# Optimization experiments

Hardware: AMD Instinct MI355X
Metric: run time of the kernel (lower is better)

## Reference

```python
import jax, jax.numpy as jnp
import numpy as np

N, L, T, D = 64, 196, 32, 512


def setup_inputs() -> dict:
    key = jax.random.key(0)
    ks = jax.random.split(key, 12)
    s = 1.0 / np.sqrt(D)
    return {
        "feature_1": jax.random.normal(ks[0], (N, L, D), jnp.float32),
        "feature_2": jax.random.normal(ks[1], (N, T, D), jnp.float32),
        "w_att": jax.random.normal(ks[2], (D,), jnp.float32) * s,
        "b_att": jnp.zeros((), jnp.float32),
        "n1_w1": jax.random.normal(ks[3], (D, D), jnp.float32) * s,
        "n1_b1": jnp.zeros((D,), jnp.float32),
        "n1_w2": jax.random.normal(ks[4], (D, D), jnp.float32) * s,
        "n1_b2": jnp.zeros((D,), jnp.float32),
        "n2_w1": jax.random.normal(ks[5], (D, D), jnp.float32) * s,
        "n2_b1": jnp.zeros((D,), jnp.float32),
        "n2_w2": jax.random.normal(ks[6], (D, D), jnp.float32) * s,
        "n2_b2": jnp.zeros((D,), jnp.float32),
    }


def _glu(x, w1, b1, w2, b2):
    # tanh(Linear1(x)) * sigmoid(Linear2(x))
    return jnp.tanh(x @ w1 + b1) * jax.nn.sigmoid(x @ w2 + b2)


def reference(feature_1, feature_2, w_att, b_att,
              n1_w1, n1_b1, n1_w2, n1_b2,
              n2_w1, n2_b1, n2_w2, n2_b2):
    f1_emb = _glu(feature_1, n1_w1, n1_b1, n1_w2, n1_b2)  # [N,L,D]
    f2_emb = _glu(feature_2, n2_w1, n2_b1, n2_w2, n2_b2)  # [N,T,D]
    # Attention_1: fc((f1 + f2 broadcast)) == fc(f1) + fc(f2) + bias since fc is linear.
    # Avoids materializing the [N,T,L,D] intermediate while computing identical math.
    s1 = feature_1 @ w_att  # [N,L]
    s2 = feature_2 @ w_att  # [N,T]
    att_logits = s2[:, :, None] + s1[:, None, :] + b_att  # [N,T,L]
    att = jax.nn.softmax(att_logits, axis=2)
    f_hat = jnp.einsum('ntl,nld->ntd', att, feature_1)  # [N,T,D]
    return (f2_emb + f_hat, f1_emb, att)
```

## Files before the change

kernel.cpp:

```cpp
#include <hip/hip_runtime.h>
#include <hip/hip_bf16.h>
#include <cstdint>
#include <cstddef>

#define N_  64
#define L_  196
#define T_  32
#define D_  512
#define LP_ 256
#define ROWS1_ (N_ * L_)
#define ROWS2_ (N_ * T_)
#define NWG1_  ((ROWS1_ / 64) * 4)
#define NWG2_  ((ROWS2_ / 64) * 4)

typedef __attribute__((ext_vector_type(8))) short short8;
typedef __attribute__((ext_vector_type(4))) float f32x4;

__device__ inline unsigned short f2bf(float f) {
  unsigned u = __builtin_bit_cast(unsigned, f);
  u = u + 0x7FFFu + ((u >> 16) & 1u);
  return (unsigned short)(u >> 16);
}

__global__ __launch_bounds__(256)
void cvt_dots(const float* __restrict__ f1, const float* __restrict__ f2,
              const float* __restrict__ w,
              unsigned short* __restrict__ f1b, unsigned short* __restrict__ f2b,
              float* __restrict__ s1, float* __restrict__ s2) {
  int row = blockIdx.x * 4 + (threadIdx.x >> 6);
  int lane = threadIdx.x & 63;
  bool isf1 = row < ROWS1_;
  const float* src = isf1 ? (f1 + (size_t)row * D_) : (f2 + (size_t)(row - ROWS1_) * D_);
  unsigned short* dst = isf1 ? (f1b + (size_t)row * D_) : (f2b + (size_t)(row - ROWS1_) * D_);
  float4 x0 = ((const float4*)src)[lane];
  float4 x1 = ((const float4*)src)[lane + 64];
  float4 w0 = ((const float4*)w)[lane];
  float4 w1 = ((const float4*)w)[lane + 64];
  float d = x0.x * w0.x + x0.y * w0.y + x0.z * w0.z + x0.w * w0.w
          + x1.x * w1.x + x1.y * w1.y + x1.z * w1.z + x1.w * w1.w;
  ushort4 o0, o1;
  o0.x = f2bf(x0.x); o0.y = f2bf(x0.y); o0.z = f2bf(x0.z); o0.w = f2bf(x0.w);
  o1.x = f2bf(x1.x); o1.y = f2bf(x1.y); o1.z = f2bf(x1.z); o1.w = f2bf(x1.w);
  ((ushort4*)dst)[lane] = o0;
  ((ushort4*)dst)[lane + 64] = o1;
  #pragma unroll
  for (int s = 32; s; s >>= 1) d += __shfl_xor(d, s);
  if (lane == 0) {
    if (isf1) s1[row] = d; else s2[row - ROWS1_] = d;
  }
}

__global__ __launch_bounds__(256)
void wt_cvt(const float* __restrict__ w0, const float* __restrict__ w1,
            const float* __restrict__ w2, const float* __restrict__ w3,
            unsigned short* __restrict__ o0, unsigned short* __restrict__ o1,
            unsigned short* __restrict__ o2, unsigned short* __restrict__ o3) {
  const float* W = (blockIdx.y == 0) ? w0 : (blockIdx.y == 1) ? w1 : (blockIdx.y == 2) ? w2 : w3;
  unsigned short* O = (blockIdx.y == 0) ? o0 : (blockIdx.y == 1) ? o1 : (blockIdx.y == 2) ? o2 : o3;
  int k0 = (blockIdx.x >> 3) * 64, n0 = (blockIdx.x & 7) * 64;
  __shared__ float tl[64][65];
  int t = threadIdx.x;
  #pragma unroll
  for (int i = 0; i < 16; i++) {
    int e = t + i * 256;
    int r = e >> 6, c = e & 63;
    tl[r][c] = W[(size_t)(k0 + r) * D_ + n0 + c];
  }
  __syncthreads();
  #pragma unroll
  for (int i = 0; i < 16; i++) {
    int e = t + i * 256;
    int r = e >> 6, c = e & 63;
    O[(size_t)(n0 + r) * D_ + k0 + c] = f2bf(tl[c][r]);
  }
}

__global__ __launch_bounds__(256)
void f1t_cvt(const unsigned short* __restrict__ f1b, unsigned short* __restrict__ f1t) {
  int bi = blockIdx.x;
  int n = bi >> 5, rem = bi & 31;
  int l0 = (rem >> 3) * 64, d0 = (rem & 7) * 64;
  __shared__ unsigned short tl[64][72];
  int t = threadIdx.x;
  #pragma unroll
  for (int i = 0; i < 4; i++) {
    int e = t + i * 256;
    int r = e >> 4, c4 = e & 15;
    int l = l0 + r;
    ushort4 v;
    if (l < L_) v = *(const ushort4*)&f1b[((size_t)n * L_ + l) * D_ + d0 + c4 * 4];
    else { v.x = 0; v.y = 0; v.z = 0; v.w = 0; }
    *(ushort4*)&tl[r][c4 * 4] = v;
  }
  __syncthreads();
  #pragma unroll
  for (int i = 0; i < 4; i++) {
    int e = t + i * 256;
    int r = e >> 4, c4 = e & 15;
    ushort4 o;
    o.x = tl[c4 * 4 + 0][r];
    o.y = tl[c4 * 4 + 1][r];
    o.z = tl[c4 * 4 + 2][r];
    o.w = tl[c4 * 4 + 3][r];
    *(ushort4*)&f1t[((size_t)n * D_ + d0 + r) * LP_ + l0 + c4 * 4] = o;
  }
}

__global__ __launch_bounds__(64)
void softmax_att(const float* __restrict__ s1, const float* __restrict__ s2,
                 const float* __restrict__ b_att, float* __restrict__ att,
                 unsigned short* __restrict__ attb) {
  int b = blockIdx.x;
  int n = b >> 5;
  int lane = threadIdx.x;
  float s2v = s2[b] + b_att[0];
  const float* s1n = s1 + (size_t)n * L_;
  float v[4];
  float mx = -1e30f;
  #pragma unroll
  for (int j = 0; j < 4; j++) {
    int l = lane + j * 64;
    v[j] = (l < L_) ? (s1n[l] + s2v) : -1e30f;
    mx = fmaxf(mx, v[j]);
  }
  #pragma unroll
  for (int s = 32; s; s >>= 1) mx = fmaxf(mx, __shfl_xor(mx, s));
  float sum = 0.f;
  #pragma unroll
  for (int j = 0; j < 4; j++) { v[j] = __expf(v[j] - mx); sum += v[j]; }
  #pragma unroll
  for (int s = 32; s; s >>= 1) sum += __shfl_xor(sum, s);
  float inv = 1.f / sum;
  float* an = att + (size_t)b * L_;
  unsigned short* ab = attb + (size_t)b * LP_;
  #pragma unroll
  for (int j = 0; j < 4; j++) {
    int l = lane + j * 64;
    float p = v[j] * inv;
    if (l < L_) an[l] = p;
    ab[l] = (l < L_) ? f2bf(p) : (unsigned short)0;
  }
}

__global__ __launch_bounds__(256, 3)
void glu_gemm(const unsigned short* __restrict__ Xb1, const unsigned short* __restrict__ Xb2,
              const unsigned short* __restrict__ W1t_1, const unsigned short* __restrict__ W2t_1,
              const unsigned short* __restrict__ W1t_2, const unsigned short* __restrict__ W2t_2,
              const float* __restrict__ b1_1, const float* __restrict__ b2_1,
              const float* __restrict__ b1_2, const float* __restrict__ b2_2,
              float* __restrict__ o1, float* __restrict__ o0) {
  int nwg = gridDim.x;
  int q = nwg >> 3;
  int orig = blockIdx.x;
  int bid = (orig & 7) * q + (orig >> 3);
  const unsigned short *Xb, *W1t, *W2t;
  const float *b1, *b2;
  float* out;
  if (bid < NWG1_) { Xb = Xb1; W1t = W1t_1; W2t = W2t_1; b1 = b1_1; b2 = b2_1; out = o1; }
  else { bid -= NWG1_; Xb = Xb2; W1t = W1t_2; W2t = W2t_2; b1 = b1_2; b2 = b2_2; out = o0; }
  int nt = bid & 3, mt = bid >> 2;
  int m0 = mt * 64, n0 = nt * 128;
  int t = threadIdx.x, lane = t & 63, wave = t >> 6;
  int wr = (wave >> 1) * 32, wc = (wave & 1) * 64;

  __shared__ alignas(16) unsigned short Xs[2][2048];
  __shared__ alignas(16) unsigned short Ws[2][2][4096];

  auto stage = [&](int buf, int k0) {
    {
      int c = t;
      const unsigned short* g = Xb + (size_t)(m0 + (c >> 2)) * D_ + k0 + (c & 3) * 8;
      unsigned short* l = &Xs[buf][(size_t)wave * 512];
      __builtin_amdgcn_global_load_lds((const __attribute__((address_space(1))) unsigned int*)g,
                                       (__attribute__((address_space(3))) unsigned int*)l,
                                       16, 0, 0);
    }
    #pragma unroll
    for (int w = 0; w < 2; w++) {
      const unsigned short* Wt = w ? W2t : W1t;
      #pragma unroll
      for (int i = 0; i < 2; i++) {
        int c = t + i * 256;
        const unsigned short* g = Wt + (size_t)(n0 + (c >> 2)) * D_ + k0 + (c & 3) * 8;
        unsigned short* l = &Ws[buf][w][(size_t)(wave * 64 + i * 256) * 8];
        __builtin_amdgcn_global_load_lds((const __attribute__((address_space(1))) unsigned int*)g,
                                         (__attribute__((address_space(3))) unsigned int*)l,
                                         16, 0, 0);
      }
    }
  };

  f32x4 acc1[2][4], acc2[2][4];
  #pragma unroll
  for (int i = 0; i < 2; i++)
    #pragma unroll
    for (int j = 0; j < 4; j++) { acc1[i][j] = (f32x4)(0.f); acc2[i][j] = (f32x4)(0.f); }

  stage(0, 0);
  int cur = 0;
  int arow = lane & 15, ak = (lane >> 4) * 8;
  for (int ks = 0; ks < 16; ++ks) {
    __syncthreads();
    if (ks < 15) stage(cur ^ 1, (ks + 1) * 32);
    short8 a[2], bf1[4], bf2[4];
    #pragma unroll
    for (int mf = 0; mf < 2; mf++)
      a[mf] = *(const short8*)&Xs[cur][(wr + mf * 16 + arow) * 32 + ak];
    #pragma unroll
    for (int nf = 0; nf < 4; nf++) {
      bf1[nf] = *(const short8*)&Ws[cur][0][(wc + nf * 16 + arow) * 32 + ak];
      bf2[nf] = *(const short8*)&Ws[cur][1][(wc + nf * 16 + arow) * 32 + ak];
    }
    #pragma unroll
    for (int mf = 0; mf < 2; mf++)
      #pragma unroll
      for (int nf = 0; nf < 4; nf++) {
        acc1[mf][nf] = __builtin_amdgcn_mfma_f32_16x16x32_bf16(a[mf], bf1[nf], acc1[mf][nf], 0, 0, 0);
        acc2[mf][nf] = __builtin_amdgcn_mfma_f32_16x16x32_bf16(a[mf], bf2[nf], acc2[mf][nf], 0, 0, 0);
      }
    cur ^= 1;
  }

  int crow = (lane >> 4) * 4, ccol = lane & 15;
  #pragma unroll
  for (int mf = 0; mf < 2; mf++) {
    #pragma unroll
    for (int nf = 0; nf < 4; nf++) {
      int col = n0 + wc + nf * 16 + ccol;
      float bb1 = b1[col], bb2 = b2[col];
      #pragma unroll
      for (int r = 0; r < 4; r++) {
        int row = m0 + wr + mf * 16 + crow + r;
        float z1 = acc1[mf][nf][r] + bb1;
        float z2 = acc2[mf][nf][r] + bb2;
        float th = 1.f - 2.f / (__expf(2.f * z1) + 1.f);
        float sg = 1.f / (1.f + __expf(-z2));
        out[(size_t)row * D_ + col] = th * sg;
      }
    }
  }
}

__global__ __launch_bounds__(256)
void fhat_mfma(const unsigned short* __restrict__ attb,
               const unsigned short* __restrict__ f1t,
               float* __restrict__ out0) {
  int n = blockIdx.x >> 2, dq = blockIdx.x & 3;
  int lane = threadIdx.x & 63, wave = threadIdx.x >> 6;
  int d0 = dq * 128 + wave * 32;
  int arow = lane & 15, ak = (lane >> 4) * 8;
  const unsigned short* A = attb + (size_t)n * T_ * LP_;
  const unsigned short* B = f1t + ((size_t)n * D_ + d0) * LP_;
  f32x4 acc[2][2];
  #pragma unroll
  for (int i = 0; i < 2; i++)
    #pragma unroll
    for (int j = 0; j < 2; j++) acc[i][j] = (f32x4)(0.f);
  #pragma unroll 2
  for (int kk = 0; kk < 8; kk++) {
    int k0 = kk * 32;
    short8 a[2], b[2];
    #pragma unroll
    for (int mt = 0; mt < 2; mt++)
      a[mt] = *(const short8*)&A[(size_t)(mt * 16 + arow) * LP_ + k0 + ak];
    #pragma unroll
    for (int nt2 = 0; nt2 < 2; nt2++)
      b[nt2] = *(const short8*)&B[(size_t)(nt2 * 16 + arow) * LP_ + k0 + ak];
    #pragma unroll
    for (int mt = 0; mt < 2; mt++)
      #pragma unroll
      for (int nt2 = 0; nt2 < 2; nt2++)
        acc[mt][nt2] = __builtin_amdgcn_mfma_f32_16x16x32_bf16(a[mt], b[nt2], acc[mt][nt2], 0, 0, 0);
  }
  int crow = (lane >> 4) * 4, ccol = lane & 15;
  #pragma unroll
  for (int mt = 0; mt < 2; mt++) {
    #pragma unroll
    for (int nt2 = 0; nt2 < 2; nt2++) {
      int d = d0 + nt2 * 16 + ccol;
      #pragma unroll
      for (int r = 0; r < 4; r++) {
        int tt = mt * 16 + crow + r;
        size_t idx = ((size_t)n * T_ + tt) * D_ + d;
        out0[idx] += acc[mt][nt2][r];
      }
    }
  }
}

extern "C" void kernel_launch(void* const* d_in, const int* in_sizes, int n_in,
                              void* d_out, int out_size, void* d_ws, size_t ws_size,
                              hipStream_t stream) {
  const float* f1    = (const float*)d_in[0];
  const float* f2    = (const float*)d_in[1];
  const float* w_att = (const float*)d_in[2];
  const float* b_att = (const float*)d_in[3];
  const float* n1w1  = (const float*)d_in[4];
  const float* n1b1  = (const float*)d_in[5];
  const float* n1w2  = (const float*)d_in[6];
  const float* n1b2  = (const float*)d_in[7];
  const float* n2w1  = (const float*)d_in[8];
  const float* n2b1  = (const float*)d_in[9];
  const float* n2w2  = (const float*)d_in[10];
  const float* n2b2  = (const float*)d_in[11];

  float* out0 = (float*)d_out;
  float* out1 = out0 + (size_t)N_ * T_ * D_;
  float* att  = out1 + (size_t)N_ * L_ * D_;

  char* ws = (char*)d_ws;
  auto alloc = [&](size_t bytes) { char* p = ws; ws += (bytes + 255) & ~(size_t)255; return p; };
  unsigned short* f1b   = (unsigned short*)alloc((size_t)ROWS1_ * D_ * 2);
  unsigned short* f2b   = (unsigned short*)alloc((size_t)ROWS2_ * D_ * 2);
  unsigned short* w1t_1 = (unsigned short*)alloc((size_t)D_ * D_ * 2);
  unsigned short* w2t_1 = (unsigned short*)alloc((size_t)D_ * D_ * 2);
  unsigned short* w1t_2 = (unsigned short*)alloc((size_t)D_ * D_ * 2);
  unsigned short* w2t_2 = (unsigned short*)alloc((size_t)D_ * D_ * 2);
  unsigned short* f1t   = (unsigned short*)alloc((size_t)N_ * D_ * LP_ * 2);
  unsigned short* attb  = (unsigned short*)alloc((size_t)N_ * T_ * LP_ * 2);
  float* s1 = (float*)alloc((size_t)ROWS1_ * 4);
  float* s2 = (float*)alloc((size_t)ROWS2_ * 4);

  cvt_dots<<<(ROWS1_ + ROWS2_) / 4, 256, 0, stream>>>(f1, f2, w_att, f1b, f2b, s1, s2);
  wt_cvt<<<dim3(64, 4), 256, 0, stream>>>(n1w1, n1w2, n2w1, n2w2, w1t_1, w2t_1, w1t_2, w2t_2);
  glu_gemm<<<NWG1_ + NWG2_, 256, 0, stream>>>(f1b, f2b, w1t_1, w2t_1, w1t_2, w2t_2,
                                              n1b1, n1b2, n2b1, n2b2, out1, out0);
  f1t_cvt<<<N_ * 32, 256, 0, stream>>>(f1b, f1t);
  softmax_att<<<N_ * T_, 64, 0, stream>>>(s1, s2, b_att, att, attb);
  fhat_mfma<<<N_ * 4, 256, 0, stream>>>(attb, f1t, out0);
}
```

Measured before the change: 157.9 us.

## Fuse softmax and f1 transpose into f_hat MFMA kernel; merge prep kernels

Merges the input conversion/dot kernel and the weight transpose kernel into one launch. Removes the separate f1 transpose and softmax kernels: the f_hat kernel now builds the softmax probabilities and a transposed bf16 tile of f1 in shared memory, then runs MFMA from LDS. This drops the global round trips through f1t and attb and removes two kernel launches. In exchange, softmax is recomputed by all four d-quarter blocks, and the scalar transposing LDS stores may cause bank conflicts.

```diff
diff --git a/kernel.cpp b/kernel.cpp
--- a/kernel.cpp
+++ b/kernel.cpp
@@ -7,11 +7,12 @@
 #define L_  196
 #define T_  32
 #define D_  512
-#define LP_ 256
 #define ROWS1_ (N_ * L_)
 #define ROWS2_ (N_ * T_)
 #define NWG1_  ((ROWS1_ / 64) * 4)
 #define NWG2_  ((ROWS2_ / 64) * 4)
+#define CVTB_  ((ROWS1_ + ROWS2_) / 4)
+#define BSTR   264
 
 typedef __attribute__((ext_vector_type(8))) short short8;
 typedef __attribute__((ext_vector_type(4))) float f32x4;
@@ -23,122 +24,57 @@
 }
 
 __global__ __launch_bounds__(256)
-void cvt_dots(const float* __restrict__ f1, const float* __restrict__ f2,
-              const float* __restrict__ w,
-              unsigned short* __restrict__ f1b, unsigned short* __restrict__ f2b,
-              float* __restrict__ s1, float* __restrict__ s2) {
-  int row = blockIdx.x * 4 + (threadIdx.x >> 6);
-  int lane = threadIdx.x & 63;
-  bool isf1 = row < ROWS1_;
-  const float* src = isf1 ? (f1 + (size_t)row * D_) : (f2 + (size_t)(row - ROWS1_) * D_);
-  unsigned short* dst = isf1 ? (f1b + (size_t)row * D_) : (f2b + (size_t)(row - ROWS1_) * D_);
-  float4 x0 = ((const float4*)src)[lane];
-  float4 x1 = ((const float4*)src)[lane + 64];
-  float4 w0 = ((const float4*)w)[lane];
-  float4 w1 = ((const float4*)w)[lane + 64];
-  float d = x0.x * w0.x + x0.y * w0.y + x0.z * w0.z + x0.w * w0.w
-          + x1.x * w1.x + x1.y * w1.y + x1.z * w1.z + x1.w * w1.w;
-  ushort4 o0, o1;
-  o0.x = f2bf(x0.x); o0.y = f2bf(x0.y); o0.z = f2bf(x0.z); o0.w = f2bf(x0.w);
-  o1.x = f2bf(x1.x); o1.y = f2bf(x1.y); o1.z = f2bf(x1.z); o1.w = f2bf(x1.w);
-  ((ushort4*)dst)[lane] = o0;
-  ((ushort4*)dst)[lane + 64] = o1;
-  #pragma unroll
-  for (int s = 32; s; s >>= 1) d += __shfl_xor(d, s);
-  if (lane == 0) {
-    if (isf1) s1[row] = d; else s2[row - ROWS1_] = d;
-  }
-}
-
-__global__ __launch_bounds__(256)
-void wt_cvt(const float* __restrict__ w0, const float* __restrict__ w1,
-            const float* __restrict__ w2, const float* __restrict__ w3,
-            unsigned short* __restrict__ o0, unsigned short* __restrict__ o1,
-            unsigned short* __restrict__ o2, unsigned short* __restrict__ o3) {
-  const float* W = (blockIdx.y == 0) ? w0 : (blockIdx.y == 1) ? w1 : (blockIdx.y == 2) ? w2 : w3;
-  unsigned short* O = (blockIdx.y == 0) ? o0 : (blockIdx.y == 1) ? o1 : (blockIdx.y == 2) ? o2 : o3;
-  int k0 = (blockIdx.x >> 3) * 64, n0 = (blockIdx.x & 7) * 64;
+void prep(const float* __restrict__ f1, const float* __restrict__ f2,
+          const float* __restrict__ w,
+          const float* __restrict__ w0, const float* __restrict__ w1,
+          const float* __restrict__ w2, const float* __restrict__ w3,
+          unsigned short* __restrict__ f1b, unsigned short* __restrict__ f2b,
+          float* __restrict__ s1, float* __restrict__ s2,
+          unsigned short* __restrict__ o0, unsigned short* __restrict__ o1,
+          unsigned short* __restrict__ o2, unsigned short* __restrict__ o3) {
   __shared__ float tl[64][65];
   int t = threadIdx.x;
-  #pragma unroll
-  for (int i = 0; i < 16; i++) {
-    int e = t + i * 256;
-    int r = e >> 6, c = e & 63;
-    tl[r][c] = W[(size_t)(k0 + r) * D_ + n0 + c];
-  }
-  __syncthreads();
-  #pragma unroll
-  for (int i = 0; i < 16; i++) {
-    int e = t + i * 256;
-    int r = e >> 6, c = e & 63;
-    O[(size_t)(n0 + r) * D_ + k0 + c] = f2bf(tl[c][r]);
-  }
-}
-
-__global__ __launch_bounds__(256)
-void f1t_cvt(const unsigned short* __restrict__ f1b, unsigned short* __restrict__ f1t) {
-  int bi = blockIdx.x;
-  int n = bi >> 5, rem = bi & 31;
-  int l0 = (rem >> 3) * 64, d0 = (rem & 7) * 64;
-  __shared__ unsigned short tl[64][72];
-  int t = threadIdx.x;
-  #pragma unroll
-  for (int i = 0; i < 4; i++) {
-    int e = t + i * 256;
-    int r = e >> 4, c4 = e & 15;
-    int l = l0 + r;
-    ushort4 v;
-    if (l < L_) v = *(const ushort4*)&f1b[((size_t)n * L_ + l) * D_ + d0 + c4 * 4];
-    else { v.x = 0; v.y = 0; v.z = 0; v.w = 0; }
-    *(ushort4*)&tl[r][c4 * 4] = v;
-  }
-  __syncthreads();
-  #pragma unroll
-  for (int i = 0; i < 4; i++) {
-    int e = t + i * 256;
-    int r = e >> 4, c4 = e & 15;
-    ushort4 o;
-    o.x = tl[c4 * 4 + 0][r];
-    o.y = tl[c4 * 4 + 1][r];
-    o.z = tl[c4 * 4 + 2][r];
-    o.w = tl[c4 * 4 + 3][r];
-    *(ushort4*)&f1t[((size_t)n * D_ + d0 + r) * LP_ + l0 + c4 * 4] = o;
-  }
-}
-
-__global__ __launch_bounds__(64)
-void softmax_att(const float* __restrict__ s1, const float* __restrict__ s2,
-                 const float* __restrict__ b_att, float* __restrict__ att,
-                 unsigned short* __restrict__ attb) {
-  int b = blockIdx.x;
-  int n = b >> 5;
-  int lane = threadIdx.x;
-  float s2v = s2[b] + b_att[0];
-  const float* s1n = s1 + (size_t)n * L_;
-  float v[4];
-  float mx = -1e30f;
-  #pragma unroll
-  for (int j = 0; j < 4; j++) {
-    int l = lane + j * 64;
-    v[j] = (l < L_) ? (s1n[l] + s2v) : -1e30f;
-    mx = fmaxf(mx, v[j]);
-  }
-  #pragma unroll
-  for (int s = 32; s; s >>= 1) mx = fmaxf(mx, __shfl_xor(mx, s));
-  float sum = 0.f;
-  #pragma unroll
-  for (int j = 0; j < 4; j++) { v[j] = __expf(v[j] - mx); sum += v[j]; }
-  #pragma unroll
-  for (int s = 32; s; s >>= 1) sum += __shfl_xor(sum, s);
-  float inv = 1.f / sum;
-  float* an = att + (size_t)b * L_;
-  unsigned short* ab = attb + (size_t)b * LP_;
-  #pragma unroll
-  for (int j = 0; j < 4; j++) {
-    int l = lane + j * 64;
-    float p = v[j] * inv;
-    if (l < L_) an[l] = p;
-    ab[l] = (l < L_) ? f2bf(p) : (unsigned short)0;
+  if (blockIdx.x < CVTB_) {
+    int row = blockIdx.x * 4 + (t >> 6);
+    int lane = t & 63;
+    bool isf1 = row < ROWS1_;
+    const float* src = isf1 ? (f1 + (size_t)row * D_) : (f2 + (size_t)(row - ROWS1_) * D_);
+    unsigned short* dst = isf1 ? (f1b + (size_t)row * D_) : (f2b + (size_t)(row - ROWS1_) * D_);
+    float4 x0 = ((const float4*)src)[lane];
+    float4 x1 = ((const float4*)src)[lane + 64];
+    float4 ww0 = ((const float4*)w)[lane];
+    float4 ww1 = ((const float4*)w)[lane + 64];
+    float d = x0.x * ww0.x + x0.y * ww0.y + x0.z * ww0.z + x0.w * ww0.w
+            + x1.x * ww1.x + x1.y * ww1.y + x1.z * ww1.z + x1.w * ww1.w;
+    ushort4 b0, b1v;
+    b0.x = f2bf(x0.x); b0.y = f2bf(x0.y); b0.z = f2bf(x0.z); b0.w = f2bf(x0.w);
+    b1v.x = f2bf(x1.x); b1v.y = f2bf(x1.y); b1v.z = f2bf(x1.z); b1v.w = f2bf(x1.w);
+    ((ushort4*)dst)[lane] = b0;
+    ((ushort4*)dst)[lane + 64] = b1v;
+    #pragma unroll
+    for (int s = 32; s; s >>= 1) d += __shfl_xor(d, s);
+    if (lane == 0) {
+      if (isf1) s1[row] = d; else s2[row - ROWS1_] = d;
+    }
+  } else {
+    int b2 = blockIdx.x - CVTB_;
+    int which = b2 >> 6, tile = b2 & 63;
+    const float* W = (which == 0) ? w0 : (which == 1) ? w1 : (which == 2) ? w2 : w3;
+    unsigned short* O = (which == 0) ? o0 : (which == 1) ? o1 : (which == 2) ? o2 : o3;
+    int k0 = (tile >> 3) * 64, n0 = (tile & 7) * 64;
+    #pragma unroll
+    for (int i = 0; i < 16; i++) {
+      int e = t + i * 256;
+      int r = e >> 6, c = e & 63;
+      tl[r][c] = W[(size_t)(k0 + r) * D_ + n0 + c];
+    }
+    __syncthreads();
+    #pragma unroll
+    for (int i = 0; i < 16; i++) {
+      int e = t + i * 256;
+      int r = e >> 6, c = e & 63;
+      O[(size_t)(n0 + r) * D_ + k0 + c] = f2bf(tl[c][r]);
+    }
   }
 }
 
@@ -242,15 +178,73 @@
 }
 
 __global__ __launch_bounds__(256)
-void fhat_mfma(const unsigned short* __restrict__ attb,
-               const unsigned short* __restrict__ f1t,
-               float* __restrict__ out0) {
+void fhat_fused(const float* __restrict__ s1, const float* __restrict__ s2,
+                const float* __restrict__ b_att,
+                const unsigned short* __restrict__ f1b,
+                float* __restrict__ att, float* __restrict__ out0) {
   int n = blockIdx.x >> 2, dq = blockIdx.x & 3;
-  int lane = threadIdx.x & 63, wave = threadIdx.x >> 6;
-  int d0 = dq * 128 + wave * 32;
+  int d0 = dq * 128;
+  int t = threadIdx.x, lane = t & 63, wave = t >> 6;
+  __shared__ unsigned short Ps[32 * BSTR];
+  __shared__ unsigned short Bs[128 * BSTR];
+
+  for (int e = t; e < 128 * 17; e += 256) {
+    int d = e / 17, qq = e % 17;
+    ushort4 z; z.x = 0; z.y = 0; z.z = 0; z.w = 0;
+    *(ushort4*)&Bs[d * BSTR + 196 + qq * 4] = z;
+  }
+  {
+    int c4 = t & 31;
+    int lr = t >> 5;
+    #pragma unroll
+    for (int i = 0; i < 25; i++) {
+      int l = i * 8 + lr;
+      if (l < L_) {
+        ushort4 v = *(const ushort4*)&f1b[((size_t)n * L_ + l) * D_ + d0 + c4 * 4];
+        Bs[(c4 * 4 + 0) * BSTR + l] = v.x;
+        Bs[(c4 * 4 + 1) * BSTR + l] = v.y;
+        Bs[(c4 * 4 + 2) * BSTR + l] = v.z;
+        Bs[(c4 * 4 + 3) * BSTR + l] = v.w;
+      }
+    }
+  }
+  {
+    int trow = wave * 8 + (lane >> 3);
+    int j = lane & 7;
+    float s2v = s2[n * T_ + trow] + b_att[0];
+    const float* s1n = s1 + (size_t)n * L_;
+    float v[25];
+    float mx = -1e30f;
+    #pragma unroll
+    for (int i = 0; i < 25; i++) {
+      int l = j + 8 * i;
+      v[i] = (l < L_) ? (s1n[l] + s2v) : -1e30f;
+      mx = fmaxf(mx, v[i]);
+    }
+    mx = fmaxf(mx, __shfl_xor(mx, 1));
+    mx = fmaxf(mx, __shfl_xor(mx, 2));
+    mx = fmaxf(mx, __shfl_xor(mx, 4));
+    float sum = 0.f;
+    #pragma unroll
+    for (int i = 0; i < 25; i++) { v[i] = __expf(v[i] - mx); sum += v[i]; }
+    sum += __shfl_xor(sum, 1);
+    sum += __shfl_xor(sum, 2);
+    sum += __shfl_xor(sum, 4);
+    float inv = 1.f / sum;
+    float* an = att + ((size_t)n * T_ + trow) * L_;
+    #pragma unroll
+    for (int i = 0; i < 32; i++) {
+      int l = j + 8 * i;
+      float p = (i < 25) ? v[i] * inv : 0.f;
+      bool valid = l < L_;
+      Ps[trow * BSTR + l] = valid ? f2bf(p) : (unsigned short)0;
+      if (dq == 0 && valid) an[l] = p;
+    }
+  }
+  __syncthreads();
+
+  int d0w = wave * 32;
   int arow = lane & 15, ak = (lane >> 4) * 8;
-  const unsigned short* A = attb + (size_t)n * T_ * LP_;
-  const unsigned short* B = f1t + ((size_t)n * D_ + d0) * LP_;
   f32x4 acc[2][2];
   #pragma unroll
   for (int i = 0; i < 2; i++)
@@ -262,10 +256,10 @@
     short8 a[2], b[2];
     #pragma unroll
     for (int mt = 0; mt < 2; mt++)
-      a[mt] = *(const short8*)&A[(size_t)(mt * 16 + arow) * LP_ + k0 + ak];
+      a[mt] = *(const short8*)&Ps[(mt * 16 + arow) * BSTR + k0 + ak];
     #pragma unroll
     for (int nt2 = 0; nt2 < 2; nt2++)
-      b[nt2] = *(const short8*)&B[(size_t)(nt2 * 16 + arow) * LP_ + k0 + ak];
+      b[nt2] = *(const short8*)&Bs[(d0w + nt2 * 16 + arow) * BSTR + k0 + ak];
     #pragma unroll
     for (int mt = 0; mt < 2; mt++)
       #pragma unroll
@@ -277,7 +271,7 @@
   for (int mt = 0; mt < 2; mt++) {
     #pragma unroll
     for (int nt2 = 0; nt2 < 2; nt2++) {
-      int d = d0 + nt2 * 16 + ccol;
+      int d = d0 + d0w + nt2 * 16 + ccol;
       #pragma unroll
       for (int r = 0; r < 4; r++) {
         int tt = mt * 16 + crow + r;
@@ -316,16 +310,13 @@
   unsigned short* w2t_1 = (unsigned short*)alloc((size_t)D_ * D_ * 2);
   unsigned short* w1t_2 = (unsigned short*)alloc((size_t)D_ * D_ * 2);
   unsigned short* w2t_2 = (unsigned short*)alloc((size_t)D_ * D_ * 2);
-  unsigned short* f1t   = (unsigned short*)alloc((size_t)N_ * D_ * LP_ * 2);
-  unsigned short* attb  = (unsigned short*)alloc((size_t)N_ * T_ * LP_ * 2);
   float* s1 = (float*)alloc((size_t)ROWS1_ * 4);
   float* s2 = (float*)alloc((size_t)ROWS2_ * 4);
 
-  cvt_dots<<<(ROWS1_ + ROWS2_) / 4, 256, 0, stream>>>(f1, f2, w_att, f1b, f2b, s1, s2);
-  wt_cvt<<<dim3(64, 4), 256, 0, stream>>>(n1w1, n1w2, n2w1, n2w2, w1t_1, w2t_1, w1t_2, w2t_2);
+  prep<<<CVTB_ + 256, 256, 0, stream>>>(f1, f2, w_att, n1w1, n1w2, n2w1, n2w2,
+                                        f1b, f2b, s1, s2,
+                                        w1t_1, w2t_1, w1t_2, w2t_2);
   glu_gemm<<<NWG1_ + NWG2_, 256, 0, stream>>>(f1b, f2b, w1t_1, w2t_1, w1t_2, w2t_2,
                                               n1b1, n1b2, n2b1, n2b2, out1, out0);
-  f1t_cvt<<<N_ * 32, 256, 0, stream>>>(f1b, f1t);
-  softmax_att<<<N_ * T_, 64, 0, stream>>>(s1, s2, b_att, att, attb);
-  fhat_mfma<<<N_ * 4, 256, 0, stream>>>(attb, f1t, out0);
-}
+  fhat_fused<<<N_ * 4, 256, 0, stream>>>(s1, s2, b_att, f1b, att, out0);
+}
```

Measured after the change: 144.8 us. -8.3%, faster.
